# Optimization experiments

Hardware: AMD Instinct MI355X
Metric: run time of the kernel (lower is better)

Reference implementation:

```python
import jax, jax.numpy as jnp
import numpy as np

WIN_H, WIN_W = 4, 7
WIN = WIN_H * WIN_W  # 28 sample points == feature channels
GRID_OFF = (0.0, 40.0)
SPATIAL_SCALE = 1.0 / 0.4
BN_EPS = 1e-3


def setup_inputs() -> dict:
    key = jax.random.key(0)
    ks = jax.random.split(key, 5)
    B, Cin, H, W = 4, 256, 200, 176
    Cout, N = WIN, 2048
    x = jax.random.normal(ks[0], (B, Cin, H, W), dtype=jnp.float32)
    # boxes [x, y, z, w, l, h, r] in realistic KITTI ranges
    lo = jnp.array([0.0, -40.0, -3.0, 1.5, 3.2, 1.4, -np.pi], jnp.float32)
    hi = jnp.array([70.0, 40.0, 1.0, 2.0, 4.2, 1.8, np.pi], jnp.float32)
    u = jax.random.uniform(ks[1], (B, N, 7), dtype=jnp.float32)
    guided_anchors = lo + u * (hi - lo)
    w1 = jax.random.normal(ks[2], (Cout, Cin, 3, 3), jnp.float32) * 0.02
    gamma = jnp.ones((Cout,), jnp.float32)
    beta = jnp.zeros((Cout,), jnp.float32)
    running_mean = jnp.zeros((Cout,), jnp.float32)
    running_var = jnp.ones((Cout,), jnp.float32)
    w2 = jax.random.normal(ks[3], (Cout, Cout, 1, 1), jnp.float32) * 0.05
    return dict(x=x, guided_anchors=guided_anchors, w1=w1, gamma=gamma,
                beta=beta, running_mean=running_mean, running_var=running_var, w2=w2)


def _convs(x, w1, gamma, beta, mean, var, w2):
    dn = ('NCHW', 'OIHW', 'NCHW')
    y = jax.lax.conv_general_dilated(x, w1, (1, 1), 'SAME', dimension_numbers=dn)
    scale = gamma * jax.lax.rsqrt(var + BN_EPS)
    y = y * scale[:, None, None] + (beta - mean * scale)[:, None, None]  # BN (inference)
    y = jax.nn.relu(y)
    return jax.lax.conv_general_dilated(y, w2, (1, 1), 'SAME', dimension_numbers=dn)


def _gen_sample_grid(box5):
    xg, yg, wg, lg, rg = (box5[:, i] for i in range(5))
    c = jnp.cos(rg)[:, None, None]
    s = jnp.sin(rg)[:, None, None]
    xx = (jnp.linspace(-0.5, 0.5, WIN_H)[None, :] * wg[:, None])[:, :, None]  # (N,4,1)
    yy = (jnp.linspace(-0.5, 0.5, WIN_W)[None, :] * lg[:, None])[:, None, :]  # (N,1,7)
    xpix = xx * c + yy * s + xg[:, None, None]  # (N,4,7)
    ypix = yy * c - xx * s + yg[:, None, None]  # (N,4,7)
    xs = ((jnp.transpose(xpix, (1, 2, 0)) + GRID_OFF[0]) * SPATIAL_SCALE).reshape(WIN, -1)
    ys = ((jnp.transpose(ypix, (1, 2, 0)) + GRID_OFF[1]) * SPATIAL_SCALE).reshape(WIN, -1)
    return xs, ys


def _bilinear_sample(img, xs, ys):
    # img: (C,H,W); xs, ys: (C,N) pixel coords (align_corners=True semantics,
    # zero padding outside) -> (C,N). Channel c samples at grid row c.
    C, H, W = img.shape
    x0 = jnp.floor(xs); y0 = jnp.floor(ys)
    wx = xs - x0; wy = ys - y0
    cidx = jnp.arange(C)[:, None]

    def gather(yf, xf):
        yi = yf.astype(jnp.int32); xi = xf.astype(jnp.int32)
        valid = (yf >= 0) & (yf <= H - 1) & (xf >= 0) & (xf <= W - 1)
        v = img[cidx, jnp.clip(yi, 0, H - 1), jnp.clip(xi, 0, W - 1)]
        return jnp.where(valid, v, 0.0)

    return (gather(y0, x0) * (1 - wx) * (1 - wy)
            + gather(y0, x0 + 1) * wx * (1 - wy)
            + gather(y0 + 1, x0) * (1 - wx) * wy
            + gather(y0 + 1, x0 + 1) * wx * wy)


def reference(x, guided_anchors, w1, gamma, beta, running_mean, running_var, w2):
    feat = _convs(x, w1, gamma, beta, running_mean, running_var, w2)  # (B,28,H,W)
    box5 = guided_anchors[:, :, jnp.array([0, 1, 3, 4, 6])]           # (B,N,5)
    xs, ys = jax.vmap(_gen_sample_grid)(box5)                          # (B,28,N) each
    vals = jax.vmap(_bilinear_sample)(feat, xs, ys)                    # (B,28,N)
    scores = jnp.mean(vals, axis=1)                                    # (B,N)
    return scores.reshape(-1)                                          # (B*N,)
```

## Files before the change

### kernel.cpp

```cpp
#include <hip/hip_runtime.h>
#include <hip/hip_bf16.h>

#define HH 200
#define WW 176
#define CIN 256
#define CO 28
#define BN_EPS 1e-3f

typedef __attribute__((ext_vector_type(8))) short short8;
typedef __attribute__((ext_vector_type(4))) float f32x4;

static __device__ __forceinline__ ushort f2bf(float f) {
    __hip_bfloat16 h = __float2bfloat16(f);
    return __builtin_bit_cast(ushort, h);
}

#define GLL16(g, l)                                                         \
    __builtin_amdgcn_global_load_lds(                                       \
        (const __attribute__((address_space(1))) void*)(g),                 \
        (__attribute__((address_space(3))) void*)(l), 16, 0, 0)

__global__ void prep_k(const float* __restrict__ w1, const float* __restrict__ gamma,
                       const float* __restrict__ beta, const float* __restrict__ mean,
                       const float* __restrict__ var, ushort* __restrict__ w1b,
                       float* __restrict__ shift)
{
    int idx = blockIdx.x * 256 + threadIdx.x;
    if (idx < CO) {
        float sc = gamma[idx] * rsqrtf(var[idx] + BN_EPS);
        shift[idx] = beta[idx] - mean[idx] * sc;
    }
    if (idx < 8 * 9 * 2 * 64 * 8) {
        int j   = idx & 7;
        int l   = (idx >> 3) & 63;
        int n   = (idx >> 9) & 1;
        int rem = idx >> 10;
        int t   = rem % 9;
        int h   = rem / 9;
        int co = n * 16 + (l & 15);
        int ci = h * 32 + (l >> 4) * 8 + j;
        float v = 0.f;
        if (co < CO) {
            float sc = gamma[co] * rsqrtf(var[co] + BN_EPS);
            v = w1[(co * CIN + ci) * 9 + t] * sc;
        }
        w1b[idx] = f2bf(v);
    }
}

__global__ __launch_bounds__(256, 3) void conv_mfma_k(
    const float* __restrict__ x, const ushort* __restrict__ w1b,
    const float* __restrict__ shift, float* __restrict__ y1)
{
    __shared__ uint4  sbuf[180 * 4];
    __shared__ ushort wls[2][9216];

    const int tid  = threadIdx.x;
    const int lane = tid & 63;
    const int w    = tid >> 6;

    const int NB = 11 * 25 * 4;
    const int q = NB / 8, r = NB % 8;
    const int bid  = blockIdx.x;
    const int xcd  = bid & 7;
    const int rank = bid >> 3;
    const int tile = (xcd < r ? xcd * (q + 1) : r * (q + 1) + (xcd - r) * q) + rank;

    const int tx  = tile % 11;
    const int rem = tile / 11;
    const int ty  = rem % 25;
    const int b   = rem / 25;
    const int x0  = tx * 16, y0 = ty * 8;

    const float* xb = x + (size_t)b * CIN * HH * WW;

    int  soff[3]; bool sval[3]; bool sp[3];
#pragma unroll
    for (int it = 0; it < 3; ++it) {
        int p = it * 64 + lane;
        sp[it] = p < 180;
        int rr = p / 18, cc = p - rr * 18;
        int gy = y0 + rr - 1, gx = x0 + cc - 1;
        bool v = (gy >= 0) & (gy < HH) & (gx >= 0) & (gx < WW) & sp[it];
        sval[it] = v;
        soff[it] = v ? gy * WW + gx : 0;
    }

    float pre[3][8];

    auto issue_x = [&](int h) {
        const float* pl = xb + (size_t)(h * 32 + w * 8) * (HH * WW);
#pragma unroll
        for (int it = 0; it < 3; ++it) {
            if (sp[it]) {
#pragma unroll
                for (int j = 0; j < 8; ++j)
                    pre[it][j] = pl[(size_t)j * (HH * WW) + soff[it]];
            }
        }
    };

    auto wr_x = [&]() {
#pragma unroll
        for (int it = 0; it < 3; ++it) {
            if (sp[it]) {
                int p = it * 64 + lane;
                ushort u[8];
#pragma unroll
                for (int j = 0; j < 8; ++j)
                    u[j] = sval[it] ? f2bf(pre[it][j]) : (ushort)0;
                uint4 val;
                val.x = (uint)u[0] | ((uint)u[1] << 16);
                val.y = (uint)u[2] | ((uint)u[3] << 16);
                val.z = (uint)u[4] | ((uint)u[5] << 16);
                val.w = (uint)u[6] | ((uint)u[7] << 16);
                sbuf[p * 4 + ((w + p) & 3)] = val;
            }
        }
    };

    auto gll_w = [&](int h) {
        const ushort* src = w1b + (size_t)h * 9216;
#pragma unroll
        for (int it = 0; it < 5; ++it) {
            int slot = it * 256 + w * 64;
            if (slot < 1152)
                GLL16(src + (size_t)(slot + lane) * 8, &wls[h & 1][slot * 8]);
        }
    };

    f32x4 acc[2][2];
#pragma unroll
    for (int m = 0; m < 2; ++m)
#pragma unroll
        for (int n = 0; n < 2; ++n)
            acc[m][n] = (f32x4){0.f, 0.f, 0.f, 0.f};

    auto compute = [&](int h) {
        const ushort* wp = wls[h & 1];
#pragma unroll
        for (int t = 0; t < 9; ++t) {
            const int dy = t / 3 - 1, dx = t % 3 - 1;
            short8 bfr[2];
#pragma unroll
            for (int n = 0; n < 2; ++n)
                bfr[n] = *(const short8*)&wp[(size_t)((t * 2 + n) * 64 + lane) * 8];
#pragma unroll
            for (int m = 0; m < 2; ++m) {
                int p = (2 * w + m + dy + 1) * 18 + (lane & 15) + dx + 1;
                uint4 av = sbuf[p * 4 + (((lane >> 4) + p) & 3)];
                short8 af = __builtin_bit_cast(short8, av);
                acc[m][0] = __builtin_amdgcn_mfma_f32_16x16x32_bf16(af, bfr[0], acc[m][0], 0, 0, 0);
                acc[m][1] = __builtin_amdgcn_mfma_f32_16x16x32_bf16(af, bfr[1], acc[m][1], 0, 0, 0);
            }
        }
    };

    gll_w(0);
    issue_x(0);
    wr_x();
    __syncthreads();

#pragma unroll 1
    for (int h = 0; h < 8; ++h) {
        if (h < 7) {
            gll_w(h + 1);
            issue_x(h + 1);
        }
        compute(h);
        if (h < 7) {
            __syncthreads();
            wr_x();
            __syncthreads();
        }
    }

    const int co0 = lane & 15;
    const int co1 = 16 + co0;
    const float s0 = shift[co0];
    const float s1 = (co1 < CO) ? shift[co1] : 0.f;
#pragma unroll
    for (int m = 0; m < 2; ++m) {
        int gy = y0 + 2 * w + m;
#pragma unroll
        for (int reg = 0; reg < 4; ++reg) {
            int gx = x0 + (lane >> 4) * 4 + reg;
            float* yp = y1 + ((size_t)(b * HH + gy) * WW + gx) * CO;
            float v0 = acc[m][0][reg] + s0;
            yp[co0] = v0 > 0.f ? v0 : 0.f;
            if (co1 < CO) {
                float v1 = acc[m][1][reg] + s1;
                yp[co1] = v1 > 0.f ? v1 : 0.f;
            }
        }
    }
}

__global__ __launch_bounds__(224) void sample_k(
    const float* __restrict__ y1, const float* __restrict__ ga,
    const float* __restrict__ w2, float* __restrict__ out)
{
    __shared__ float red[224];
    const int lb  = threadIdx.x / CO;
    const int k   = threadIdx.x % CO;
    const int box = blockIdx.x * 8 + lb;
    const int b   = box >> 11;

    const float* ap = ga + (size_t)box * 7;
    float xg = ap[0], yg = ap[1], wg = ap[3], lg = ap[4], rg = ap[6];
    float c = cosf(rg), s = sinf(rg);

    const int i = k / 7, j = k % 7;
    float xx = ((float)i * (1.f / 3.f) - 0.5f) * wg;
    float yy = ((float)j * (1.f / 6.f) - 0.5f) * lg;
    float xs = (xx * c + yy * s + xg) * 2.5f;
    float ys = (yy * c - xx * s + yg + 40.f) * 2.5f;

    float x0 = floorf(xs), y0 = floorf(ys);
    float wx = xs - x0,    wy = ys - y0;

    float w2r[CO];
    const float* w2p = w2 + k * CO;
#pragma unroll
    for (int q = 0; q < 7; ++q) {
        float4 t = ((const float4*)w2p)[q];
        w2r[4*q] = t.x; w2r[4*q+1] = t.y; w2r[4*q+2] = t.z; w2r[4*q+3] = t.w;
    }

    float val = 0.f;
    const float* yb = y1 + (size_t)b * HH * WW * CO;
#pragma unroll
    for (int cor = 0; cor < 4; ++cor) {
        float yf = y0 + (float)(cor >> 1);
        float xf = x0 + (float)(cor & 1);
        float cw = ((cor & 1) ? wx : 1.f - wx) * ((cor >> 1) ? wy : 1.f - wy);
        if (yf >= 0.f && yf <= (float)(HH - 1) && xf >= 0.f && xf <= (float)(WW - 1)) {
            int yi = (int)yf, xi = (int)xf;
            const float* p = yb + ((size_t)yi * WW + xi) * CO;
            float d = 0.f;
#pragma unroll
            for (int q = 0; q < 7; ++q) {
                float4 t = ((const float4*)p)[q];
                d = fmaf(w2r[4*q],   t.x, d);
                d = fmaf(w2r[4*q+1], t.y, d);
                d = fmaf(w2r[4*q+2], t.z, d);
                d = fmaf(w2r[4*q+3], t.w, d);
            }
            val = fmaf(cw, d, val);
        }
    }

    red[threadIdx.x] = val;
    __syncthreads();
    if (k == 0) {
        float sum = 0.f;
#pragma unroll
        for (int q = 0; q < CO; ++q) sum += red[lb * CO + q];
        out[box] = sum * (1.f / 28.f);
    }
}

extern "C" void kernel_launch(void* const* d_in, const int* in_sizes, int n_in,
                              void* d_out, int out_size, void* d_ws, size_t ws_size,
                              hipStream_t stream) {
    const float* x     = (const float*)d_in[0];
    const float* ga    = (const float*)d_in[1];
    const float* w1    = (const float*)d_in[2];
    const float* gamma = (const float*)d_in[3];
    const float* beta  = (const float*)d_in[4];
    const float* mean  = (const float*)d_in[5];
    const float* var   = (const float*)d_in[6];
    const float* w2    = (const float*)d_in[7];
    float* out = (float*)d_out;

    ushort* w1b   = (ushort*)d_ws;
    float*  shift = (float*)((char*)d_ws + 147456);
    float*  y1    = (float*)((char*)d_ws + 147968);

    prep_k<<<(8 * 9 * 2 * 64 * 8 + 255) / 256, 256, 0, stream>>>(
        w1, gamma, beta, mean, var, w1b, shift);

    conv_mfma_k<<<11 * 25 * 4, 256, 0, stream>>>(x, w1b, shift, y1);

    sample_k<<<(4 * 2048) / 8, 224, 0, stream>>>(y1, ga, w2, out);
}
```

Measured before the change: 76.26 us.

## Load conv weights directly to registers and double-buffer input tile in LDS

Result: slower. 86.49 us (+13.4%).

```diff
diff --git a/kernel.cpp b/kernel.cpp
--- a/kernel.cpp
+++ b/kernel.cpp
@@ -14,11 +14,6 @@
     __hip_bfloat16 h = __float2bfloat16(f);
     return __builtin_bit_cast(ushort, h);
 }
-
-#define GLL16(g, l)                                                         \
-    __builtin_amdgcn_global_load_lds(                                       \
-        (const __attribute__((address_space(1))) void*)(g),                 \
-        (__attribute__((address_space(3))) void*)(l), 16, 0, 0)
 
 __global__ void prep_k(const float* __restrict__ w1, const float* __restrict__ gamma,
                        const float* __restrict__ beta, const float* __restrict__ mean,
@@ -52,8 +47,7 @@
     const float* __restrict__ x, const ushort* __restrict__ w1b,
     const float* __restrict__ shift, float* __restrict__ y1)
 {
-    __shared__ uint4  sbuf[180 * 4];
-    __shared__ ushort wls[2][9216];
+    __shared__ uint4 sbuf[2][180 * 4];
 
     const int tid  = threadIdx.x;
     const int lane = tid & 63;
@@ -100,7 +94,7 @@
         }
     };
 
-    auto wr_x = [&]() {
+    auto wr_x = [&](int bi) {
 #pragma unroll
         for (int it = 0; it < 3; ++it) {
             if (sp[it]) {
@@ -114,18 +108,8 @@
                 val.y = (uint)u[2] | ((uint)u[3] << 16);
                 val.z = (uint)u[4] | ((uint)u[5] << 16);
                 val.w = (uint)u[6] | ((uint)u[7] << 16);
-                sbuf[p * 4 + ((w + p) & 3)] = val;
-            }
-        }
-    };
-
-    auto gll_w = [&](int h) {
-        const ushort* src = w1b + (size_t)h * 9216;
-#pragma unroll
-        for (int it = 0; it < 5; ++it) {
-            int slot = it * 256 + w * 64;
-            if (slot < 1152)
-                GLL16(src + (size_t)(slot + lane) * 8, &wls[h & 1][slot * 8]);
+                sbuf[bi][p * 4 + ((w + p) & 3)] = val;
+            }
         }
     };
 
@@ -136,41 +120,50 @@
         for (int n = 0; n < 2; ++n)
             acc[m][n] = (f32x4){0.f, 0.f, 0.f, 0.f};
 
-    auto compute = [&](int h) {
-        const ushort* wp = wls[h & 1];
-#pragma unroll
-        for (int t = 0; t < 9; ++t) {
-            const int dy = t / 3 - 1, dx = t % 3 - 1;
-            short8 bfr[2];
-#pragma unroll
-            for (int n = 0; n < 2; ++n)
-                bfr[n] = *(const short8*)&wp[(size_t)((t * 2 + n) * 64 + lane) * 8];
-#pragma unroll
-            for (int m = 0; m < 2; ++m) {
-                int p = (2 * w + m + dy + 1) * 18 + (lane & 15) + dx + 1;
-                uint4 av = sbuf[p * 4 + (((lane >> 4) + p) & 3)];
-                short8 af = __builtin_bit_cast(short8, av);
-                acc[m][0] = __builtin_amdgcn_mfma_f32_16x16x32_bf16(af, bfr[0], acc[m][0], 0, 0, 0);
-                acc[m][1] = __builtin_amdgcn_mfma_f32_16x16x32_bf16(af, bfr[1], acc[m][1], 0, 0, 0);
-            }
-        }
-    };
-
-    gll_w(0);
     issue_x(0);
-    wr_x();
+    wr_x(0);
     __syncthreads();
 
 #pragma unroll 1
     for (int h = 0; h < 8; ++h) {
+        short8 wreg[9][2];
+        {
+            const ushort* wsrc = w1b + (size_t)h * 9216;
+#pragma unroll
+            for (int t = 0; t < 9; ++t)
+#pragma unroll
+                for (int n = 0; n < 2; ++n)
+                    wreg[t][n] = *(const short8*)(wsrc + (size_t)((t * 2 + n) * 64 + lane) * 8);
+        }
+        if (h < 7) issue_x(h + 1);
+        __builtin_amdgcn_sched_barrier(0);
+
+        {
+            const uint4* sb = sbuf[h & 1];
+            short8 av[4][3];
+#pragma unroll
+            for (int rr = 0; rr < 4; ++rr) {
+#pragma unroll
+                for (int dx = 0; dx < 3; ++dx) {
+                    int p = (2 * w + rr) * 18 + (lane & 15) + dx;
+                    av[rr][dx] = __builtin_bit_cast(short8, sb[p * 4 + (((lane >> 4) + p) & 3)]);
+                }
+            }
+#pragma unroll
+            for (int t = 0; t < 9; ++t) {
+                const int dy = t / 3, dx = t % 3;
+#pragma unroll
+                for (int m = 0; m < 2; ++m) {
+                    short8 af = av[m + dy][dx];
+                    acc[m][0] = __builtin_amdgcn_mfma_f32_16x16x32_bf16(af, wreg[t][0], acc[m][0], 0, 0, 0);
+                    acc[m][1] = __builtin_amdgcn_mfma_f32_16x16x32_bf16(af, wreg[t][1], acc[m][1], 0, 0, 0);
+                }
+            }
+        }
+        __builtin_amdgcn_sched_barrier(0);
+
         if (h < 7) {
-            gll_w(h + 1);
-            issue_x(h + 1);
-        }
-        compute(h);
-        if (h < 7) {
-            __syncthreads();
-            wr_x();
+            wr_x((h + 1) & 1);
             __syncthreads();
         }
     }
```
